# Kernel tuning notes

Measured on AMD Instinct MI355X. Metric: run time of the kernel, lower is better.

Reference implementation:

```python
import jax, jax.numpy as jnp
import numpy as np

B, D, T, H, K = 16, 1024, 1024, 1024, 2  # batch, in_channels, seq_len, hidden_size, kernel_size


def setup_inputs() -> dict:
    key = jax.random.key(0)
    k1, k2, k3 = jax.random.split(key, 3)
    inputs = jax.random.normal(k1, (B, D, T), dtype=jnp.float32)
    # Conv1D kernel in OIH layout: [3H, D, K]; scaled to keep gates in a sane range
    conv_w = jax.random.normal(k2, (3 * H, D, K), dtype=jnp.float32) / np.float32(np.sqrt(D * K))
    conv_b = jax.random.normal(k3, (3 * H,), dtype=jnp.float32) * 0.01
    return {"inputs": inputs, "conv_w": conv_w, "conv_b": conv_b}


def reference(inputs, conv_w, conv_b):
    # inputs: [B, D, T] (channels_first, as in the keras call signature)
    # Causal conv: left-pad time by K-1, then VALID conv -> [B, 3H, T]
    padded = jnp.pad(inputs, ((0, 0), (0, 0), (K - 1, 0)))
    gates = jax.lax.conv_general_dilated(
        padded, conv_w, window_strides=(1,), padding="VALID",
        dimension_numbers=("NCH", "OIH", "NCH"))
    gates = gates + conv_b[None, :, None]
    gates = jnp.transpose(gates, (0, 2, 1))  # [B, T, 3H]
    z = jnp.tanh(gates[..., :H])
    f = jax.nn.sigmoid(gates[..., H:2 * H])
    o = jax.nn.sigmoid(gates[..., 2 * H:])

    # fo-pooling linear recurrence: c_t = f_t * c_{t-1} + (1 - f_t) * z_t, c_0 = 0
    zf = (jnp.transpose(z, (1, 0, 2)), jnp.transpose(f, (1, 0, 2)))  # time-major [T, B, H]

    def step(c, zf_t):
        z_t, f_t = zf_t
        c_new = f_t * c + (1.0 - f_t) * z_t
        return c_new, c_new

    c0 = jnp.zeros((B, H), dtype=inputs.dtype)
    _, c_seq = jax.lax.scan(step, c0, zf)
    c_seq = jnp.transpose(c_seq, (1, 0, 2))  # [B, T, H]
    h_seq = o * c_seq
    return c_seq, h_seq
```

## Files before the change

### kernel.cpp

```cpp
#include <hip/hip_runtime.h>

#define Bsz 16
#define Dch 1024
#define Tsz 1024
#define Hsz 1024
#define Mtot (Bsz*Tsz)
#define K2   (2*Dch)
#define Ntot (3*Hsz)
#define NCH  16
#define CL   64

typedef __attribute__((ext_vector_type(8))) short bf16x8;
typedef __attribute__((ext_vector_type(4))) float f32x4;

__device__ __forceinline__ unsigned short f2bf(float x) {
    unsigned u = __float_as_uint(x);
    u += 0x7FFFu + ((u >> 16) & 1u);
    return (unsigned short)(u >> 16);
}
__device__ __forceinline__ float bf2f(unsigned short s) {
    return __uint_as_float(((unsigned)s) << 16);
}

#define GLOAD_LDS16(gp, lp) \
    __builtin_amdgcn_global_load_lds((const __attribute__((address_space(1))) void*)(gp), \
                                     (__attribute__((address_space(3))) void*)(lp), 16, 0, 0)

__global__ __launch_bounds__(256)
void prep(const float* __restrict__ x, unsigned short* __restrict__ a2,
          const float* __restrict__ w, unsigned short* __restrict__ wb) {
    __shared__ float Xs[64][66];
    int bid = blockIdx.x;
    int tid = threadIdx.x;
    if (bid >= 4096) {
        int i0 = (bid - 4096) * 256 + tid;
        #pragma unroll
        for (int k = 0; k < 4; k++) {
            int i = i0 + k * (1536 * 256);
            float4 v = ((const float4*)w)[i];
            ushort4 r;
            r.x = f2bf(v.x); r.y = f2bf(v.y); r.z = f2bf(v.z); r.w = f2bf(v.w);
            ((ushort4*)wb)[i] = r;
        }
        return;
    }
    int b   = bid >> 8;
    int tt0 = ((bid >> 4) & 15) << 6;
    int dd0 = (bid & 15) << 6;
    int colt = tid & 63, rowq = tid >> 6;
    const size_t xbase = (size_t)b * (Dch * Tsz);
    #pragma unroll
    for (int r = 0; r < 16; r++) {
        int dd = r * 4 + rowq;
        Xs[dd][1 + colt] = x[xbase + (size_t)(dd0 + dd) * Tsz + tt0 + colt];
    }
    if (tid < 64) {
        Xs[tid][0] = (tt0 == 0) ? 0.f : x[xbase + (size_t)(dd0 + tid) * Tsz + tt0 - 1];
    }
    __syncthreads();
    #pragma unroll
    for (int r = 0; r < 16; r++) {
        int tr = r * 4 + rowq;
        int dc = colt;
        float v0 = Xs[dc][tr];
        float v1 = Xs[dc][tr + 1];
        unsigned pack = (unsigned)f2bf(v0) | ((unsigned)f2bf(v1) << 16);
        int m = (b << 10) + tt0 + tr;
        ((unsigned*)a2)[(size_t)m * (K2 / 2) + dd0 + dc] = pack;
    }
}

__global__ __launch_bounds__(256)
void gemm_gates(const unsigned short* __restrict__ A, const unsigned short* __restrict__ Bt,
                const float* __restrict__ bias,
                float* __restrict__ zc, float* __restrict__ fh, unsigned short* __restrict__ ob) {
    __shared__ __align__(16) unsigned short As[128 * 64];
    __shared__ __align__(16) unsigned short Bs2[128 * 64];
    int tid = threadIdx.x;
    int n0 = blockIdx.x << 7;
    int m0 = blockIdx.y << 7;
    int wave = tid >> 6, lane = tid & 63;
    int wm = wave & 1, wn = wave >> 1;
    int lm = lane & 15, q = lane >> 4;

    int lrow = lane >> 3, lchunk = lane & 7;
    int gch  = lchunk ^ lrow;
    const unsigned short* Ag = A  + (size_t)(m0 + wave * 32 + lrow) * K2 + gch * 8;
    const unsigned short* Bg = Bt + (size_t)(n0 + wave * 32 + lrow) * K2 + gch * 8;

    f32x4 acc[4][4] = {};
    for (int kb = 0; kb < K2; kb += 64) {
        #pragma unroll
        for (int j = 0; j < 4; j++) {
            int rbase = wave * 32 + j * 8;
            GLOAD_LDS16(Ag + (size_t)j * 8 * K2 + kb, &As[rbase * 64]);
            GLOAD_LDS16(Bg + (size_t)j * 8 * K2 + kb, &Bs2[rbase * 64]);
        }
        __syncthreads();
        #pragma unroll
        for (int ks = 0; ks < 64; ks += 32) {
            bf16x8 af[4], bfr[4];
            int cs = ks >> 3;
            int sw = (lm & 7);
            #pragma unroll
            for (int i = 0; i < 4; i++)
                af[i] = *(bf16x8*)&As[(wm * 64 + i * 16 + lm) * 64 + (((cs + q) ^ sw) << 3)];
            #pragma unroll
            for (int j = 0; j < 4; j++)
                bfr[j] = *(bf16x8*)&Bs2[(wn * 64 + j * 16 + lm) * 64 + (((cs + q) ^ sw) << 3)];
            #pragma unroll
            for (int i = 0; i < 4; i++)
                #pragma unroll
                for (int j = 0; j < 4; j++)
                    acc[i][j] = __builtin_amdgcn_mfma_f32_16x16x32_bf16(af[i], bfr[j], acc[i][j], 0, 0, 0);
        }
        __syncthreads();
    }
    int gt = n0 >> 10;
    #pragma unroll
    for (int i = 0; i < 4; i++) {
        int mrow = m0 + wm * 64 + i * 16 + q * 4;
        #pragma unroll
        for (int j = 0; j < 4; j++) {
            int n = n0 + wn * 64 + j * 16 + lm;
            float bv = bias[n];
            int hcol = n & 1023;
            #pragma unroll
            for (int r = 0; r < 4; r++) {
                float g = acc[i][j][r] + bv;
                size_t idx = (size_t)(mrow + r) * Hsz + hcol;
                if (gt == 0) {
                    float e = __expf(2.f * g);
                    zc[idx] = __fdividef(e - 1.f, e + 1.f);
                } else {
                    float s = __fdividef(1.f, 1.f + __expf(-g));
                    if (gt == 1) fh[idx] = s;
                    else         ob[idx] = f2bf(s);
                }
            }
        }
    }
}

__global__ __launch_bounds__(256)
void scan1(const float* __restrict__ zc, const float* __restrict__ fh,
           float* __restrict__ Aw, float* __restrict__ Bw) {
    int blk = blockIdx.x;
    int hb = blk & 1, ch = (blk >> 1) & 15, b = blk >> 5;
    int h = hb * 512 + threadIdx.x * 2;
    size_t base = ((size_t)b << 20) + ((size_t)(ch * CL) << 10) + h;
    float ax = 1.f, ay = 1.f, bx = 0.f, by = 0.f;
    #pragma unroll 8
    for (int s = 0; s < CL; s++) {
        size_t idx = base + ((size_t)s << 10);
        float2 z = *(const float2*)&zc[idx];
        float2 f = *(const float2*)&fh[idx];
        ax *= f.x; ay *= f.y;
        bx = z.x + f.x * (bx - z.x);
        by = z.y + f.y * (by - z.y);
    }
    int o = (ch * Bsz + b) * Hsz + h;
    *(float2*)&Aw[o] = make_float2(ax, ay);
    *(float2*)&Bw[o] = make_float2(bx, by);
}

__global__ __launch_bounds__(256)
void scan3(float* __restrict__ zc, float* __restrict__ fh,
           const unsigned short* __restrict__ ob,
           const float* __restrict__ Aw, const float* __restrict__ Bw) {
    int blk = blockIdx.x;
    int hb = blk & 1, ch = (blk >> 1) & 15, b = blk >> 5;
    int h = hb * 512 + threadIdx.x * 2;
    float cx = 0.f, cy = 0.f;
    for (int cp = 0; cp < ch; cp++) {
        int o = (cp * Bsz + b) * Hsz + h;
        float2 A = *(const float2*)&Aw[o];
        float2 B = *(const float2*)&Bw[o];
        cx = A.x * cx + B.x;
        cy = A.y * cy + B.y;
    }
    size_t base = ((size_t)b << 20) + ((size_t)(ch * CL) << 10) + h;
    #pragma unroll 8
    for (int s = 0; s < CL; s++) {
        size_t idx = base + ((size_t)s << 10);
        float2 z = *(const float2*)&zc[idx];
        float2 f = *(const float2*)&fh[idx];
        unsigned ov = *(const unsigned*)&ob[idx];
        cx = z.x + f.x * (cx - z.x);
        cy = z.y + f.y * (cy - z.y);
        *(float2*)&zc[idx] = make_float2(cx, cy);
        float ox = bf2f((unsigned short)(ov & 0xFFFF));
        float oy = bf2f((unsigned short)(ov >> 16));
        *(float2*)&fh[idx] = make_float2(ox * cx, oy * cy);
    }
}

extern "C" void kernel_launch(void* const* d_in, const int* in_sizes, int n_in,
                              void* d_out, int out_size, void* d_ws, size_t ws_size,
                              hipStream_t stream) {
    const float* x    = (const float*)d_in[0];
    const float* w    = (const float*)d_in[1];
    const float* bias = (const float*)d_in[2];
    float* zc = (float*)d_out;
    float* fh = (float*)d_out + (size_t)Mtot * Hsz;
    unsigned short* a2 = (unsigned short*)d_ws;
    unsigned short* wb = a2 + (size_t)Mtot * K2;
    unsigned short* ob = wb + (size_t)Ntot * K2;
    float* Aw = (float*)(ob + (size_t)Mtot * Hsz);
    float* Bw = Aw + NCH * Bsz * Hsz;

    hipLaunchKernelGGL(prep, dim3(5632), dim3(256), 0, stream, x, a2, w, wb);
    hipLaunchKernelGGL(gemm_gates, dim3(24, 128), dim3(256), 0, stream, a2, wb, bias, zc, fh, ob);
    hipLaunchKernelGGL(scan1, dim3(512), dim3(256), 0, stream, zc, fh, Aw, Bw);
    hipLaunchKernelGGL(scan3, dim3(512), dim3(256), 0, stream, zc, fh, ob, Aw, Bw);
}
```

Measured before the change: 507.7 us.

## Rewrite gate GEMM as 256x256 double-buffered pipelined MFMA kernel with tile swizzle

Replaces the 128x128 single-buffered GEMM with 256x256 tiles computed by 8 waves. LDS is double-buffered and global-to-LDS loads for later k-steps are interleaved with MFMA phases using explicit waitcnt, barriers, sched_barrier and setprio. Block IDs are remapped so neighbouring blocks share tiles in cache. The aim is to hide load latency and raise MFMA utilisation in the dominant GEMM. The cost is 128KB of LDS, heavy register pressure from 8x4 accumulators, and fragile hand-written waitcnt ordering.

```diff
diff --git a/kernel.cpp b/kernel.cpp
--- a/kernel.cpp
+++ b/kernel.cpp
@@ -9,6 +9,7 @@
 #define Ntot (3*Hsz)
 #define NCH  16
 #define CL   64
+#define NT   32
 
 typedef __attribute__((ext_vector_type(8))) short bf16x8;
 typedef __attribute__((ext_vector_type(4))) float f32x4;
@@ -70,63 +71,144 @@
     }
 }
 
-__global__ __launch_bounds__(256)
+#define MFMA_PAIR(i0) do { \
+    _Pragma("unroll") for (int ks_ = 0; ks_ < 2; ++ks_) { \
+      _Pragma("unroll") for (int di_ = 0; di_ < 2; ++di_) { \
+        _Pragma("unroll") for (int j_ = 0; j_ < 4; ++j_) { \
+          acc[(i0)+di_][j_] = __builtin_amdgcn_mfma_f32_16x16x32_bf16( \
+              af[(i0)+di_][ks_], bfr[ks_][j_], acc[(i0)+di_][j_], 0, 0, 0); \
+        } } } } while (0)
+
+__global__ __launch_bounds__(512, 2)
 void gemm_gates(const unsigned short* __restrict__ A, const unsigned short* __restrict__ Bt,
                 const float* __restrict__ bias,
                 float* __restrict__ zc, float* __restrict__ fh, unsigned short* __restrict__ ob) {
-    __shared__ __align__(16) unsigned short As[128 * 64];
-    __shared__ __align__(16) unsigned short Bs2[128 * 64];
-    int tid = threadIdx.x;
-    int n0 = blockIdx.x << 7;
-    int m0 = blockIdx.y << 7;
-    int wave = tid >> 6, lane = tid & 63;
-    int wm = wave & 1, wn = wave >> 1;
-    int lm = lane & 15, q = lane >> 4;
-
-    int lrow = lane >> 3, lchunk = lane & 7;
-    int gch  = lchunk ^ lrow;
-    const unsigned short* Ag = A  + (size_t)(m0 + wave * 32 + lrow) * K2 + gch * 8;
-    const unsigned short* Bg = Bt + (size_t)(n0 + wave * 32 + lrow) * K2 + gch * 8;
-
-    f32x4 acc[4][4] = {};
-    for (int kb = 0; kb < K2; kb += 64) {
-        #pragma unroll
-        for (int j = 0; j < 4; j++) {
-            int rbase = wave * 32 + j * 8;
-            GLOAD_LDS16(Ag + (size_t)j * 8 * K2 + kb, &As[rbase * 64]);
-            GLOAD_LDS16(Bg + (size_t)j * 8 * K2 + kb, &Bs2[rbase * 64]);
-        }
-        __syncthreads();
-        #pragma unroll
-        for (int ks = 0; ks < 64; ks += 32) {
-            bf16x8 af[4], bfr[4];
-            int cs = ks >> 3;
-            int sw = (lm & 7);
-            #pragma unroll
-            for (int i = 0; i < 4; i++)
-                af[i] = *(bf16x8*)&As[(wm * 64 + i * 16 + lm) * 64 + (((cs + q) ^ sw) << 3)];
-            #pragma unroll
-            for (int j = 0; j < 4; j++)
-                bfr[j] = *(bf16x8*)&Bs2[(wn * 64 + j * 16 + lm) * 64 + (((cs + q) ^ sw) << 3)];
-            #pragma unroll
-            for (int i = 0; i < 4; i++)
-                #pragma unroll
-                for (int j = 0; j < 4; j++)
-                    acc[i][j] = __builtin_amdgcn_mfma_f32_16x16x32_bf16(af[i], bfr[j], acc[i][j], 0, 0, 0);
-        }
-        __syncthreads();
-    }
-    int gt = n0 >> 10;
+    __shared__ __align__(16) unsigned short As[2][16384];
+    __shared__ __align__(16) unsigned short Bs[2][16384];
+
+    int tid  = threadIdx.x;
+    int wv   = tid >> 6, lane = tid & 63;
+    int wm   = wv >> 2, wn = wv & 3;
+    int lm   = lane & 15, q = lane >> 4;
+
+    int bid = blockIdx.x;
+    int swz = (bid & 7) * 96 + (bid >> 3);
+    int mt = swz / 12, nt = swz % 12;
+    int m0 = mt << 8, n0 = nt << 8;
+
+    const unsigned short* Abase = A  + (size_t)m0 * K2;
+    const unsigned short* Bbase = Bt + (size_t)n0 * K2;
+
+    int loff   = (wv * 8 + (lane >> 3)) * K2 + (((lane & 7) ^ (lane >> 3)) << 3);
+    int ldsoff = wv * 8 * 64;
+
+    int sw  = lm & 7;
+    int kc0 = (q ^ sw) << 3;
+    int kc1 = ((4 + q) ^ sw) << 3;
+    int aoff = (wm * 128 + lm) * 64;
+    int boff = (wn * 64 + lm) * 64;
+
+    f32x4 acc[8][4] = {};
+    bf16x8 af[8][2], bfr[2][4];
+
+#define STAGE_A(t, h) do { \
+    const unsigned short* g_ = Abase + (h) * (128 * K2) + (t) * 64 + loff; \
+    unsigned short* l_ = &As[(t) & 1][(h) * 8192 + ldsoff]; \
+    GLOAD_LDS16(g_, l_); \
+    GLOAD_LDS16(g_ + 64 * K2, l_ + 64 * 64); } while (0)
+#define STAGE_B(t, h) do { \
+    const unsigned short* g_ = Bbase + (h) * (128 * K2) + (t) * 64 + loff; \
+    unsigned short* l_ = &Bs[(t) & 1][(h) * 8192 + ldsoff]; \
+    GLOAD_LDS16(g_, l_); \
+    GLOAD_LDS16(g_ + 64 * K2, l_ + 64 * 64); } while (0)
+
+    STAGE_A(0, 0); STAGE_A(0, 1); STAGE_B(0, 0); STAGE_B(0, 1);
+    STAGE_B(1, 1); STAGE_B(1, 0); STAGE_A(1, 0);
+    asm volatile("s_waitcnt vmcnt(6)" ::: "memory");
+    __builtin_amdgcn_s_barrier();
+
+    #pragma unroll 2
+    for (int t = 0; t < NT; ++t) {
+        const unsigned short* Ab = As[t & 1];
+        const unsigned short* Bb = Bs[t & 1];
+
+        #pragma unroll
+        for (int j = 0; j < 4; ++j) {
+            bfr[0][j] = *(const bf16x8*)&Bb[boff + j * 1024 + kc0];
+            bfr[1][j] = *(const bf16x8*)&Bb[boff + j * 1024 + kc1];
+        }
+        #pragma unroll
+        for (int i = 0; i < 2; ++i) {
+            af[i][0] = *(const bf16x8*)&Ab[aoff + i * 1024 + kc0];
+            af[i][1] = *(const bf16x8*)&Ab[aoff + i * 1024 + kc1];
+        }
+        if (t + 1 < NT) STAGE_A(t + 1, 1);
+        asm volatile("s_waitcnt lgkmcnt(8)" ::: "memory");
+        __builtin_amdgcn_sched_barrier(0);
+        __builtin_amdgcn_s_barrier();
+        asm volatile("s_waitcnt lgkmcnt(0)" ::: "memory");
+        __builtin_amdgcn_sched_barrier(0);
+        __builtin_amdgcn_s_setprio(1);
+        MFMA_PAIR(0);
+        __builtin_amdgcn_s_setprio(0);
+        __builtin_amdgcn_sched_barrier(0);
+        __builtin_amdgcn_s_barrier();
+
+        #pragma unroll
+        for (int i = 2; i < 4; ++i) {
+            af[i][0] = *(const bf16x8*)&Ab[aoff + i * 1024 + kc0];
+            af[i][1] = *(const bf16x8*)&Ab[aoff + i * 1024 + kc1];
+        }
+        if (t + 2 < NT) STAGE_B(t + 2, 1);
+        __builtin_amdgcn_sched_barrier(0);
+        __builtin_amdgcn_s_barrier();
+        asm volatile("s_waitcnt lgkmcnt(0)" ::: "memory");
+        __builtin_amdgcn_sched_barrier(0);
+        __builtin_amdgcn_s_setprio(1);
+        MFMA_PAIR(2);
+        __builtin_amdgcn_s_setprio(0);
+        __builtin_amdgcn_sched_barrier(0);
+        __builtin_amdgcn_s_barrier();
+
+        #pragma unroll
+        for (int i = 4; i < 8; ++i) {
+            af[i][0] = *(const bf16x8*)&Ab[aoff + i * 1024 + kc0];
+            af[i][1] = *(const bf16x8*)&Ab[aoff + i * 1024 + kc1];
+        }
+        if (t + 2 < NT) STAGE_B(t + 2, 0);
+        __builtin_amdgcn_sched_barrier(0);
+        __builtin_amdgcn_s_barrier();
+        asm volatile("s_waitcnt lgkmcnt(0)" ::: "memory");
+        __builtin_amdgcn_sched_barrier(0);
+        __builtin_amdgcn_s_setprio(1);
+        MFMA_PAIR(4);
+        __builtin_amdgcn_s_setprio(0);
+        __builtin_amdgcn_sched_barrier(0);
+        __builtin_amdgcn_s_barrier();
+
+        if (t + 2 < NT) STAGE_A(t + 2, 0);
+        __builtin_amdgcn_sched_barrier(0);
+        __builtin_amdgcn_s_barrier();
+        __builtin_amdgcn_s_setprio(1);
+        MFMA_PAIR(6);
+        __builtin_amdgcn_s_setprio(0);
+        __builtin_amdgcn_sched_barrier(0);
+        if (t < NT - 2)       asm volatile("s_waitcnt vmcnt(6)" ::: "memory");
+        else if (t == NT - 2) asm volatile("s_waitcnt vmcnt(0)" ::: "memory");
+        __builtin_amdgcn_s_barrier();
+    }
+
+    int gt = nt >> 2;
     #pragma unroll
-    for (int i = 0; i < 4; i++) {
-        int mrow = m0 + wm * 64 + i * 16 + q * 4;
-        #pragma unroll
-        for (int j = 0; j < 4; j++) {
+    for (int i = 0; i < 8; ++i) {
+        int mrow = m0 + wm * 128 + i * 16 + q * 4;
+        #pragma unroll
+        for (int j = 0; j < 4; ++j) {
             int n = n0 + wn * 64 + j * 16 + lm;
             float bv = bias[n];
             int hcol = n & 1023;
             #pragma unroll
-            for (int r = 0; r < 4; r++) {
+            for (int r = 0; r < 4; ++r) {
                 float g = acc[i][j][r] + bv;
                 size_t idx = (size_t)(mrow + r) * Hsz + hcol;
                 if (gt == 0) {
@@ -210,7 +292,7 @@
     float* Bw = Aw + NCH * Bsz * Hsz;
 
     hipLaunchKernelGGL(prep, dim3(5632), dim3(256), 0, stream, x, a2, w, wb);
-    hipLaunchKernelGGL(gemm_gates, dim3(24, 128), dim3(256), 0, stream, a2, wb, bias, zc, fh, ob);
+    hipLaunchKernelGGL(gemm_gates, dim3(768), dim3(512), 0, stream, a2, wb, bias, zc, fh, ob);
     hipLaunchKernelGGL(scan1, dim3(512), dim3(256), 0, stream, zc, fh, Aw, Bw);
     hipLaunchKernelGGL(scan3, dim3(512), dim3(256), 0, stream, zc, fh, ob, Aw, Bw);
 }
```

New measurement: 466.0 us. 8.2% less time.
